# Kernel tuning notes

Hardware: AMD Instinct MI355X
Metric: run time of the kernel (lower is better)

## Reference

```python
import jax, jax.numpy as jnp
import numpy as np

B, N, E, D, H, HW, L = 16, 32, 256, 256, 8, 784, 4
DH = D // H
FF = 4 * D
BN = B * N
BE = B * E
SCALE = 1.0 / np.sqrt(DH)


def _ln(x, g, b):
    m = x.mean(-1, keepdims=True)
    v = ((x - m) ** 2).mean(-1, keepdims=True)
    return (x - m) * jax.lax.rsqrt(v + 1e-5) * g + b


def setup_inputs() -> dict:
    key = jax.random.key(0)
    ks = iter(jax.random.split(key, 64))
    def w(shape, s=0.05):
        return jax.random.normal(next(ks), shape, jnp.float32) * s
    inp = {
        'nodes': w((B, N, D), 1.0),
        'edges': w((B, E, D), 1.0),
        'images': w((B, HW, D), 1.0),
        'mask': jnp.zeros((B * H, N + E, HW), jnp.float32),
        'node_enc': w((BN, D), 1.0),
        'edge_enc': w((BE, D), 1.0),
        'ln1_g': jnp.ones((L, D), jnp.float32), 'ln1_b': jnp.zeros((L, D), jnp.float32),
        'Wqkv': w((L, D, 3 * D)), 'bqkv': jnp.zeros((L, 3 * D), jnp.float32),
        'Wo': w((L, D, D)), 'bo': jnp.zeros((L, D), jnp.float32),
        'ls1': jnp.full((L, D), 0.1, jnp.float32),
        'ln2_g': jnp.ones((L, D), jnp.float32), 'ln2_b': jnp.zeros((L, D), jnp.float32),
        'Wn1': w((L, D, D)), 'bn1': jnp.zeros((L, D), jnp.float32),
        'Wn2': w((L, D, D)), 'bn2': jnp.zeros((L, D), jnp.float32),
        'We': w((L, D, D)), 'be': jnp.zeros((L, D), jnp.float32),
        'attn_p': w((L, H, DH), 1.0),
        'Weo': w((L, D, D)), 'beo': jnp.zeros((L, D), jnp.float32),
        'Wno': w((L, D, D)), 'bno': jnp.zeros((L, D), jnp.float32),
        'ls2': jnp.full((L, D), 0.1, jnp.float32),
        'ln3_g': jnp.ones((L, D), jnp.float32), 'ln3_b': jnp.zeros((L, D), jnp.float32),
        'W1': w((L, D, FF)), 'b1': jnp.zeros((L, FF), jnp.float32),
        'W2': w((L, FF, D)), 'b2': jnp.zeros((L, D), jnp.float32),
        'ls3': jnp.full((L, D), 0.1, jnp.float32),
        'edge_index': jax.random.randint(next(ks), (2, BE), 0, BN, jnp.int32),
    }
    return inp


def reference(nodes, edges, images, mask, node_enc, edge_enc,
              ln1_g, ln1_b, Wqkv, bqkv, Wo, bo, ls1,
              ln2_g, ln2_b, Wn1, bn1, Wn2, bn2, We, be, attn_p, Weo, beo, Wno, bno, ls2,
              ln3_g, ln3_b, W1, b1, W2, b2, ls3, edge_index):
    idx0, idx1 = edge_index[0], edge_index[1]
    ne = jnp.concatenate([nodes, edges], axis=1)  # [B, N+E, D]
    mask4 = mask.reshape(B, H, N + E, HW)
    for l in range(L):
        # cross-attention ne -> images
        ne1n = _ln(ne, ln1_g[l], ln1_b[l])
        q = (ne1n @ Wqkv[l, :, :D] + bqkv[l, :D]).reshape(B, N + E, H, DH)
        k = (images @ Wqkv[l, :, D:2 * D] + bqkv[l, D:2 * D]).reshape(B, HW, H, DH)
        v = (images @ Wqkv[l, :, 2 * D:] + bqkv[l, 2 * D:]).reshape(B, HW, H, DH)
        scores = jnp.einsum('bqhd,bkhd->bhqk', q, k) * SCALE + mask4
        attn = jax.nn.softmax(scores, axis=-1)
        ctx = jnp.einsum('bhqk,bkhd->bqhd', attn, v).reshape(B, N + E, D)
        ne1 = ne + ls1[l] * (ctx @ Wo[l] + bo[l])
        # modified GAT on flattened graph
        ne2n = _ln(ne1, ln2_g[l], ln2_b[l])
        nodes_f = ne2n[:, :N].reshape(BN, D) + node_enc
        edges_f = ne2n[:, N:].reshape(BE, D) + edge_enc
        fn = (nodes_f @ Wn1[l] + bn1[l])[idx0]
        sn = (nodes_f @ Wn2[l] + bn2[l])[idx0]  # NOTE: original code uses edge_index[0] here too
        ep = edges_f @ We[l] + be[l]
        hidden = jax.nn.gelu(fn + sn + ep, approximate=False)  # [BE, D]
        pres = (hidden.reshape(BE, H, DH) * attn_p[l]).sum(-1)  # [BE, H]
        mseg = jax.ops.segment_max(pres, idx0, num_segments=BN)
        expv = jnp.exp(pres - mseg[idx0])
        denom = jax.ops.segment_sum(expv, idx0, num_segments=BN)
        alpha = expv / denom[idx0]  # scatter_softmax over destination nodes
        new_edges = hidden @ Weo[l] + beo[l]
        vals = (nodes_f[idx1] + new_edges) @ Wno[l] + bno[l]
        vals = vals.reshape(BE, H, DH) * alpha[..., None]
        new_nodes = jax.ops.segment_sum(vals.reshape(BE, D), idx0, num_segments=BN)
        gat = jnp.concatenate([new_nodes.reshape(B, N, D), new_edges.reshape(B, E, D)], axis=1)
        ne2 = ne1 + ls2[l] * gat
        # FFN
        ne3n = _ln(ne2, ln3_g[l], ln3_b[l])
        ffn = jax.nn.gelu(ne3n @ W1[l] + b1[l], approximate=False) @ W2[l] + b2[l]
        ne = ne2 + ls3[l] * ffn
    return ne
```

## Files before the change

kernel.cpp:

```cpp
#include <hip/hip_runtime.h>
#include <math.h>

static constexpr int B_  = 16;
static constexpr int N_  = 32;
static constexpr int E_  = 256;
static constexpr int D_  = 256;
static constexpr int H_  = 8;
static constexpr int HW_ = 784;
static constexpr int L_  = 4;
static constexpr int DH_ = 32;
static constexpr int FF_ = 1024;
static constexpr int BN_ = 512;
static constexpr int BE_ = 4096;
static constexpr int NE_ = 288;
#define SCALE_ 0.17677669529663687f

static constexpr size_t LAYER_W = 1114112;
static constexpr size_t OFF_Q   = 0;
static constexpr size_t OFF_K   = 65536;
static constexpr size_t OFF_V   = 131072;
static constexpr size_t OFF_WO  = 196608;
static constexpr size_t OFF_WN1 = 262144;
static constexpr size_t OFF_WN2 = 327680;
static constexpr size_t OFF_WE  = 393216;
static constexpr size_t OFF_WEO = 458752;
static constexpr size_t OFF_WNO = 524288;
static constexpr size_t OFF_W1  = 589824;
static constexpr size_t OFF_W2  = 851968;

typedef __attribute__((ext_vector_type(8))) short bf16x8;
typedef __attribute__((ext_vector_type(4))) float f32x4;

__device__ __forceinline__ float gelu_f(float x) {
    return 0.5f * x * (1.0f + erff(x * 0.7071067811865476f));
}

__device__ __forceinline__ unsigned short f2bf(float x) {
    unsigned u = __float_as_uint(x);
    u += 0x7FFFu + ((u >> 16) & 1u);
    return (unsigned short)(u >> 16);
}
__device__ __forceinline__ unsigned pack2bf(float a, float b) {
    return (unsigned)f2bf(a) | ((unsigned)f2bf(b) << 16);
}
__device__ __forceinline__ float bf2f(unsigned short u) {
    return __uint_as_float(((unsigned)u) << 16);
}


__global__ void concat_kernel(const float* __restrict__ nodes, const float* __restrict__ edges,
                              float* __restrict__ ne) {
    int tid = blockIdx.x * 256 + threadIdx.x;
    int d = tid & 255;
    int row = tid >> 8;
    int b = row / NE_, pos = row % NE_;
    float v = (pos < N_) ? nodes[(size_t)(b * N_ + pos) * D_ + d]
                         : edges[(size_t)(b * E_ + (pos - N_)) * D_ + d];
    ne[tid] = v;
}

__global__ void imgcast_kernel(const float* __restrict__ img, unsigned short* __restrict__ out) {
    int tid = blockIdx.x * 256 + threadIdx.x;
    const float* p = img + (size_t)tid * 8;
    float4 a = *(const float4*)(p);
    float4 b = *(const float4*)(p + 4);
    uint4 o = make_uint4(pack2bf(a.x, a.y), pack2bf(a.z, a.w),
                         pack2bf(b.x, b.y), pack2bf(b.z, b.w));
    *(uint4*)&out[(size_t)tid * 8] = o;
}

__device__ __forceinline__ float ln_row_val(const float* __restrict__ x, int row, int d,
                                            const float* __restrict__ g, const float* __restrict__ bta,
                                            float* sh1, float* sh2) {
    float v = x[(size_t)row * D_ + d];
    float s = v, s2 = v * v;
    #pragma unroll
    for (int o = 32; o >= 1; o >>= 1) { s += __shfl_down(s, o); s2 += __shfl_down(s2, o); }
    int lane = d & 63, w = d >> 6;
    if (lane == 0) { sh1[w] = s; sh2[w] = s2; }
    __syncthreads();
    if (d == 0) {
        float a = sh1[0] + sh1[1] + sh1[2] + sh1[3];
        float c = sh2[0] + sh2[1] + sh2[2] + sh2[3];
        sh1[0] = a; sh2[0] = c;
    }
    __syncthreads();
    float mean = sh1[0] * (1.0f / D_);
    float var  = sh2[0] * (1.0f / D_) - mean * mean;
    float rstd = rsqrtf(var + 1e-5f);
    return (v - mean) * rstd * g[d] + bta[d];
}

__global__ __launch_bounds__(256) void ln_kernel(const float* __restrict__ x,
                                                 unsigned short* __restrict__ y,
                                                 const float* __restrict__ g,
                                                 const float* __restrict__ bta) {
    __shared__ float sh1[4], sh2[4];
    const int row = blockIdx.x, d = threadIdx.x;
    float val = ln_row_val(x, row, d, g, bta, sh1, sh2);
    y[(size_t)row * D_ + d] = f2bf(val);
}

__global__ __launch_bounds__(256) void ln2enc_kernel(const float* __restrict__ x,
                                                     const float* __restrict__ g,
                                                     const float* __restrict__ bta,
                                                     const float* __restrict__ node_enc,
                                                     const float* __restrict__ edge_enc,
                                                     unsigned short* __restrict__ nodes_f,
                                                     unsigned short* __restrict__ edges_f) {
    __shared__ float sh1[4], sh2[4];
    const int row = blockIdx.x, d = threadIdx.x;
    float val = ln_row_val(x, row, d, g, bta, sh1, sh2);
    int b = row / NE_, pos = row % NE_;
    if (pos < N_) {
        int rn = b * N_ + pos;
        nodes_f[(size_t)rn * D_ + d] = f2bf(val + node_enc[(size_t)rn * D_ + d]);
    } else {
        int re = b * E_ + (pos - N_);
        edges_f[(size_t)re * D_ + d] = f2bf(val + edge_enc[(size_t)re * D_ + d]);
    }
}

__global__ __launch_bounds__(256) void wtrans_kernel(
    const float* __restrict__ Wqkv, const float* __restrict__ Wo,
    const float* __restrict__ Wn1,  const float* __restrict__ Wn2,
    const float* __restrict__ We,   const float* __restrict__ Weo,
    const float* __restrict__ Wno,  const float* __restrict__ W1,
    const float* __restrict__ W2,   unsigned short* __restrict__ wT)
{
    const int bid = blockIdx.x;
    const int l = bid / 1088;
    int tl = bid % 1088;
    const float* src; int ld, K, Nn; unsigned short* dst;
    if (tl < 576) {
        int mid = tl >> 6; tl &= 63;
        K = 256; Nn = 256;
        if (mid < 3) {
            src = Wqkv + (size_t)l * 256 * 768 + mid * 256; ld = 768;
            dst = wT + (size_t)l * LAYER_W + (size_t)mid * 65536;
        } else {
            const float* bases[6] = {Wo, Wn1, Wn2, We, Weo, Wno};
            src = bases[mid - 3] + (size_t)l * 65536; ld = 256;
            dst = wT + (size_t)l * LAYER_W + OFF_WO + (size_t)(mid - 3) * 65536;
        }
    } else if (tl < 832) {
        tl -= 576; K = 256; Nn = 1024;
        src = W1 + (size_t)l * 262144; ld = 1024;
        dst = wT + (size_t)l * LAYER_W + OFF_W1;
    } else {
        tl -= 832; K = 1024; Nn = 256;
        src = W2 + (size_t)l * 262144; ld = 256;
        dst = wT + (size_t)l * LAYER_W + OFF_W2;
    }
    const int ntn = Nn >> 5;
    const int k0 = (tl / ntn) << 5, n0 = (tl % ntn) << 5;
    __shared__ float ts[32][33];
    const int t = threadIdx.x;
    const int kl = t >> 5, nl = t & 31;
    #pragma unroll
    for (int rr = 0; rr < 4; ++rr)
        ts[kl + rr * 8][nl] = src[(size_t)(k0 + kl + rr * 8) * ld + n0 + nl];
    __syncthreads();
    const int onl = t >> 3, okl = (t & 7) << 2;
    ushort4 o;
    o.x = f2bf(ts[okl + 0][onl]); o.y = f2bf(ts[okl + 1][onl]);
    o.z = f2bf(ts[okl + 2][onl]); o.w = f2bf(ts[okl + 3][onl]);
    *(ushort4*)&dst[(size_t)(n0 + onl) * K + k0 + okl] = o;
}

template<int MODE, int OUTBF>
__global__ __launch_bounds__(256) void mgemm_kernel(
    const unsigned short* __restrict__ A, int lda,
    const unsigned short* __restrict__ Bt,
    const float* __restrict__ bias,
    const float* __restrict__ res,
    const float* __restrict__ ls,
    void* __restrict__ Cv, int ldc, int K)
{
    __shared__ unsigned short As[64][72];
    __shared__ unsigned short Bs[64][72];
    const int m0 = blockIdx.y * 64, n0 = blockIdx.x * 64;
    const int t = threadIdx.x;
    const int l = t & 63, w = t >> 6;
    const int wr = (w >> 1) * 32, wc = (w & 1) * 32;
    const int srow = t >> 2, skc = (t & 3) * 16;
    const int frow = l & 15, kg = l >> 4;
    f32x4 acc[2][2];
    acc[0][0] = (f32x4){0.f,0.f,0.f,0.f}; acc[0][1] = acc[0][0];
    acc[1][0] = acc[0][0];                acc[1][1] = acc[0][0];
    for (int k0 = 0; k0 < K; k0 += 64) {
        const unsigned short* ap = A + (size_t)(m0 + srow) * lda + k0 + skc;
        uint4 aq0 = *(const uint4*)(ap);
        uint4 aq1 = *(const uint4*)(ap + 8);
        const unsigned short* bp = Bt + (size_t)(n0 + srow) * K + k0 + skc;
        uint4 bq0 = *(const uint4*)(bp);
        uint4 bq1 = *(const uint4*)(bp + 8);
        __syncthreads();
        *(uint4*)&As[srow][skc]     = aq0;
        *(uint4*)&As[srow][skc + 8] = aq1;
        *(uint4*)&Bs[srow][skc]     = bq0;
        *(uint4*)&Bs[srow][skc + 8] = bq1;
        __syncthreads();
        #pragma unroll
        for (int kk = 0; kk < 2; ++kk) {
            bf16x8 af0 = *(const bf16x8*)&As[wr + frow][kk * 32 + kg * 8];
            bf16x8 af1 = *(const bf16x8*)&As[wr + 16 + frow][kk * 32 + kg * 8];
            bf16x8 bf0 = *(const bf16x8*)&Bs[wc + frow][kk * 32 + kg * 8];
            bf16x8 bf1 = *(const bf16x8*)&Bs[wc + 16 + frow][kk * 32 + kg * 8];
            acc[0][0] = __builtin_amdgcn_mfma_f32_16x16x32_bf16(af0, bf0, acc[0][0], 0, 0, 0);
            acc[0][1] = __builtin_amdgcn_mfma_f32_16x16x32_bf16(af0, bf1, acc[0][1], 0, 0, 0);
            acc[1][0] = __builtin_amdgcn_mfma_f32_16x16x32_bf16(af1, bf0, acc[1][0], 0, 0, 0);
            acc[1][1] = __builtin_amdgcn_mfma_f32_16x16x32_bf16(af1, bf1, acc[1][1], 0, 0, 0);
        }
    }
    #pragma unroll
    for (int fr = 0; fr < 2; ++fr) {
        #pragma unroll
        for (int fc = 0; fc < 2; ++fc) {
            int n = n0 + wc + fc * 16 + frow;
            float bv = bias[n];
            float lv = (MODE == 2) ? ls[n] : 0.f;
            #pragma unroll
            for (int rg = 0; rg < 4; ++rg) {
                int m = m0 + wr + fr * 16 + kg * 4 + rg;
                float vv = acc[fr][fc][rg] + bv;
                if (MODE == 1) vv = gelu_f(vv);
                if (MODE == 2) vv = res[(size_t)m * ldc + n] + lv * vv;
                if (OUTBF) ((unsigned short*)Cv)[(size_t)m * ldc + n] = f2bf(vv);
                else       ((float*)Cv)[(size_t)m * ldc + n] = vv;
            }
        }
    }
}

__global__ __launch_bounds__(128) void attn_kernel(
    const unsigned short* __restrict__ q, const unsigned short* __restrict__ kv,
    const float* __restrict__ mask, unsigned short* __restrict__ ctx)
{
    const int bid = blockIdx.x;
    const int h = bid & 7;
    const int qt = (bid >> 3) % 9;
    const int b = (bid >> 3) / 9;
    const int q0 = qt * 32;
    const int t = threadIdx.x;
    const int w = t >> 6, l = t & 63;
    const int lr = l & 15, lg = l >> 4;
    constexpr int NC = (HW_ + 63) / 64;

    __shared__ unsigned short Ks[2][64][40];
    __shared__ unsigned short Vs[2][32][72];
    __shared__ unsigned short Pl[2][16][72];

    bf16x8 qfrag = *(const bf16x8*)(q + ((size_t)(b * NE_ + q0 + w * 16 + lr)) * D_ + h * DH_ + lg * 8);

    const int kkey = t >> 1, kdh = (t & 1) * 16;
    const int vdh = (t & 7) * 4, vk0 = (t >> 3) * 2;
    const unsigned short* kbase = kv + ((size_t)b * HW_) * 512 + h * DH_;
    const unsigned short* vbase = kv + ((size_t)b * HW_) * 512 + 256 + h * DH_;
    const float* mbase = mask + ((size_t)(b * H_ + h) * NE_ + q0 + w * 16 + lg * 4) * (size_t)HW_;

    uint4 kq0, kq1;
    ushort4 va[2], vb4[2];
    float mreg[4][4];

    auto issue_kv = [&](int c0) {
        {
            int key = c0 + kkey;
            bool ok = key < HW_;
            const unsigned short* kp = kbase + (size_t)(ok ? key : 0) * 512 + kdh;
            kq0 = *(const uint4*)(kp);
            kq1 = *(const uint4*)(kp + 8);
            if (!ok) { kq0 = make_uint4(0,0,0,0); kq1 = kq0; }
        }
        #pragma unroll
        for (int r = 0; r < 2; ++r) {
            int key = c0 + vk0 + 32 * r;
            bool ok0 = key < HW_, ok1 = (key + 1) < HW_;
            const unsigned short* vp = vbase + (size_t)(ok0 ? key : 0) * 512 + vdh;
            va[r]  = *(const ushort4*)(vp);
            vb4[r] = *(const ushort4*)(vp + (ok1 ? 512 : 0));
            if (!ok0) va[r]  = make_ushort4(0,0,0,0);
            if (!ok1) vb4[r] = make_ushort4(0,0,0,0);
        }
    };
    auto write_kv = [&](int bufi) {
        *(uint4*)&Ks[bufi][kkey][kdh]     = kq0;
        *(uint4*)&Ks[bufi][kkey][kdh + 8] = kq1;
        #pragma unroll
        for (int r = 0; r < 2; ++r) {
            const unsigned short* a = (const unsigned short*)&va[r];
            const unsigned short* c = (const unsigned short*)&vb4[r];
            #pragma unroll
            for (int i = 0; i < 4; ++i)
                *(unsigned*)&Vs[bufi][vdh + i][vk0 + 32 * r] = (unsigned)a[i] | ((unsigned)c[i] << 16);
        }
    };
    auto issue_mask = [&](int c0) {
        #pragma unroll
        for (int rg = 0; rg < 4; ++rg)
            #pragma unroll
            for (int fc = 0; fc < 4; ++fc) {
                int col = c0 + fc * 16 + lr;
                mreg[rg][fc] = (col < HW_) ? mbase[(size_t)rg * HW_ + col] : -1e30f;
            }
    };

    f32x4 oacc[2];
    oacc[0] = (f32x4){0.f, 0.f, 0.f, 0.f}; oacc[1] = oacc[0];
    float m_i[4] = {-INFINITY, -INFINITY, -INFINITY, -INFINITY};
    float l_i[4] = {0.f, 0.f, 0.f, 0.f};

    issue_kv(0);
    write_kv(0);
    issue_mask(0);
    __syncthreads();

    for (int c = 0; c < NC; ++c) {
        const int c0 = c * 64;
        const int cb = c & 1, nb = cb ^ 1;
        if (c + 1 < NC) issue_kv(c0 + 64);

        f32x4 sacc[4];
        #pragma unroll
        for (int fc = 0; fc < 4; ++fc) {
            sacc[fc] = (f32x4){0.f, 0.f, 0.f, 0.f};
            bf16x8 kf = *(const bf16x8*)&Ks[cb][fc * 16 + lr][lg * 8];
            sacc[fc] = __builtin_amdgcn_mfma_f32_16x16x32_bf16(qfrag, kf, sacc[fc], 0, 0, 0);
        }
        float s[4][4];
        #pragma unroll
        for (int fc = 0; fc < 4; ++fc)
            #pragma unroll
            for (int rg = 0; rg < 4; ++rg)
                s[fc][rg] = sacc[fc][rg] * SCALE_ + mreg[rg][fc];
        if (c + 1 < NC) issue_mask(c0 + 64);

        float mloc[4];
        #pragma unroll
        for (int rg = 0; rg < 4; ++rg)
            mloc[rg] = fmaxf(fmaxf(s[0][rg], s[1][rg]), fmaxf(s[2][rg], s[3][rg]));
        #pragma unroll
        for (int off = 1; off < 16; off <<= 1)
            #pragma unroll
            for (int rg = 0; rg < 4; ++rg)
                mloc[rg] = fmaxf(mloc[rg], __shfl_xor(mloc[rg], off));
        float scl[4], lloc[4];
        #pragma unroll
        for (int rg = 0; rg < 4; ++rg) {
            float mn = fmaxf(m_i[rg], mloc[rg]);
            scl[rg] = __expf(m_i[rg] - mn);
            m_i[rg] = mn;
        }
        #pragma unroll
        for (int rg = 0; rg < 4; ++rg) {
            float acc = 0.f;
            #pragma unroll
            for (int fc = 0; fc < 4; ++fc) {
                float p = __expf(s[fc][rg] - m_i[rg]);
                s[fc][rg] = p;
                acc += p;
            }
            lloc[rg] = acc;
        }
        #pragma unroll
        for (int off = 1; off < 16; off <<= 1)
            #pragma unroll
            for (int rg = 0; rg < 4; ++rg)
                lloc[rg] += __shfl_xor(lloc[rg], off);
        #pragma unroll
        for (int rg = 0; rg < 4; ++rg) {
            l_i[rg] = l_i[rg] * scl[rg] + lloc[rg];
            oacc[0][rg] *= scl[rg];
            oacc[1][rg] *= scl[rg];
        }

        #pragma unroll
        for (int fc = 0; fc < 4; ++fc)
            #pragma unroll
            for (int rg = 0; rg < 4; ++rg)
                Pl[w][lg * 4 + rg][fc * 16 + lr] = f2bf(s[fc][rg]);
        #pragma unroll
        for (int ks2 = 0; ks2 < 2; ++ks2) {
            bf16x8 pf = *(const bf16x8*)&Pl[w][lr][ks2 * 32 + lg * 8];
            #pragma unroll
            for (int d2 = 0; d2 < 2; ++d2) {
                bf16x8 vf = *(const bf16x8*)&Vs[cb][d2 * 16 + lr][ks2 * 32 + lg * 8];
                oacc[d2] = __builtin_amdgcn_mfma_f32_16x16x32_bf16(pf, vf, oacc[d2], 0, 0, 0);
            }
        }

        if (c + 1 < NC) {
            write_kv(nb);
            __syncthreads();
        }
    }

    unsigned short* cbase = ctx + ((size_t)(b * NE_ + q0 + w * 16 + lg * 4)) * D_ + h * DH_;
    #pragma unroll
    for (int rg = 0; rg < 4; ++rg) {
        float inv = 1.0f / l_i[rg];
        #pragma unroll
        for (int d2 = 0; d2 < 2; ++d2)
            cbase[(size_t)rg * D_ + d2 * 16 + lr] = f2bf(oacc[d2][rg] * inv);
    }
}


__global__ __launch_bounds__(256) void hidden_kernel(
    const float* __restrict__ gn1, const float* __restrict__ gn2,
    unsigned short* __restrict__ hid, const int* __restrict__ idx0,
    const float* __restrict__ attn_p_l, float* __restrict__ pres) {
    int e = blockIdx.x;
    int d = threadIdx.x;
    int n = idx0[e];
    float x = bf2f(hid[(size_t)e * D_ + d]) + gn1[(size_t)n * D_ + d] + gn2[(size_t)n * D_ + d];
    float hv = gelu_f(x);
    hid[(size_t)e * D_ + d] = f2bf(hv);
    float pr = hv * attn_p_l[d];
    #pragma unroll
    for (int o = 1; o < 32; o <<= 1) pr += __shfl_xor(pr, o);
    if ((d & 31) == 0) pres[e * H_ + (d >> 5)] = pr;
}

__global__ void segsoft_kernel(const float* __restrict__ pres, const int* __restrict__ csr_off,
                               const int* __restrict__ csr_perm,
                               float* __restrict__ mseg, float* __restrict__ denom) {
    int tid = blockIdx.x * 256 + threadIdx.x;
    int n = tid >> 3, h = tid & 7;
    int s = csr_off[n], e2 = csr_off[n + 1];
    float mx = -INFINITY;
    for (int i = s; i < e2; ++i) mx = fmaxf(mx, pres[csr_perm[i] * H_ + h]);
    float sum = 0.f;
    for (int i = s; i < e2; ++i) sum += expf(pres[csr_perm[i] * H_ + h] - mx);
    mseg[tid] = mx;
    denom[tid] = sum;
}

__global__ void alpha_kernel(const float* __restrict__ pres, const int* __restrict__ idx0,
                             const float* __restrict__ mseg, const float* __restrict__ denom,
                             float* __restrict__ alpha) {
    int tid = blockIdx.x * 256 + threadIdx.x;
    int e = tid >> 3, h = tid & 7;
    int n = idx0[e];
    alpha[tid] = expf(pres[tid] - mseg[n * H_ + h]) / denom[n * H_ + h];
}

__global__ void vin_kernel(const unsigned short* __restrict__ nodes_f,
                           const float* __restrict__ new_edges,
                           const int* __restrict__ idx1, unsigned short* __restrict__ vin) {
    int tid = blockIdx.x * 256 + threadIdx.x;
    int e = tid >> 8, d = tid & 255;
    vin[tid] = f2bf(bf2f(nodes_f[(size_t)idx1[e] * D_ + d]) + new_edges[tid]);
}

__global__ __launch_bounds__(256) void nodeagg_kernel(
    const float* __restrict__ vals, const float* __restrict__ alpha,
    const int* __restrict__ csr_off, const int* __restrict__ csr_perm,
    float* __restrict__ new_nodes) {
    int n = blockIdx.x;
    int d = threadIdx.x;
    int s = csr_off[n], e2 = csr_off[n + 1];
    int h = d >> 5;
    float acc = 0.f;
    for (int i = s; i < e2; ++i) {
        int e = csr_perm[i];
        acc += vals[(size_t)e * D_ + d] * alpha[e * H_ + h];
    }
    new_nodes[(size_t)n * D_ + d] = acc;
}

__global__ void gatres_kernel(float* __restrict__ ne, const float* __restrict__ new_nodes,
                              const float* __restrict__ new_edges, const float* __restrict__ ls2l) {
    int tid = blockIdx.x * 256 + threadIdx.x;
    int d = tid & 255;
    int row = tid >> 8;
    int b = row / NE_, pos = row % NE_;
    float g = (pos < N_) ? new_nodes[(size_t)(b * N_ + pos) * D_ + d]
                         : new_edges[(size_t)(b * E_ + (pos - N_)) * D_ + d];
    ne[tid] += ls2l[d] * g;
}


__global__ void zero_counts(int* counts) {
    int t = blockIdx.x * 256 + threadIdx.x;
    if (t < BN_) counts[t] = 0;
}

__global__ void csr_count(const int* __restrict__ idx0, int* __restrict__ counts) {
    int e = blockIdx.x * 256 + threadIdx.x;
    if (e < BE_) atomicAdd(&counts[idx0[e]], 1);
}

__global__ __launch_bounds__(512) void csr_scan(const int* __restrict__ counts, int* __restrict__ csr_off) {
    __shared__ int buf[BN_];
    int t = threadIdx.x;
    int c = counts[t];
    buf[t] = c;
    __syncthreads();
    for (int o = 1; o < BN_; o <<= 1) {
        int add = (t >= o) ? buf[t - o] : 0;
        __syncthreads();
        buf[t] += add;
        __syncthreads();
    }
    csr_off[t] = buf[t] - c;
    if (t == BN_ - 1) csr_off[BN_] = buf[t];
}

__global__ __launch_bounds__(64) void csr_fill(const int* __restrict__ idx0,
                                               const int* __restrict__ csr_off,
                                               int* __restrict__ csr_perm) {
    int n = blockIdx.x;
    int lane = threadIdx.x;
    int w = csr_off[n];
    for (int c0 = 0; c0 < BE_; c0 += 64) {
        int e = c0 + lane;
        bool m = (idx0[e] == n);
        unsigned long long bal = __ballot(m);
        if (m) {
            int pre = __popcll(bal & ((1ull << lane) - 1ull));
            csr_perm[w + pre] = e;
        }
        w += __popcll(bal);
    }
}


static void launch_mgemm(hipStream_t s, int mode, int outbf,
                         const unsigned short* A, int lda, const unsigned short* Bt,
                         const float* bias, const float* res, const float* ls,
                         void* C, int ldc, int M, int N, int K) {
    dim3 g(N / 64, M / 64);
    if (mode == 0) {
        if (outbf) mgemm_kernel<0,1><<<g, 256, 0, s>>>(A, lda, Bt, bias, res, ls, C, ldc, K);
        else       mgemm_kernel<0,0><<<g, 256, 0, s>>>(A, lda, Bt, bias, res, ls, C, ldc, K);
    } else if (mode == 1) {
        mgemm_kernel<1,1><<<g, 256, 0, s>>>(A, lda, Bt, bias, res, ls, C, ldc, K);
    } else {
        mgemm_kernel<2,0><<<g, 256, 0, s>>>(A, lda, Bt, bias, res, ls, C, ldc, K);
    }
}

extern "C" void kernel_launch(void* const* d_in, const int* in_sizes, int n_in,
                              void* d_out, int out_size, void* d_ws, size_t ws_size,
                              hipStream_t stream) {
    const float* nodes    = (const float*)d_in[0];
    const float* edges    = (const float*)d_in[1];
    const float* images   = (const float*)d_in[2];
    const float* mask     = (const float*)d_in[3];
    const float* node_enc = (const float*)d_in[4];
    const float* edge_enc = (const float*)d_in[5];
    const float* ln1_g = (const float*)d_in[6];
    const float* ln1_b = (const float*)d_in[7];
    const float* Wqkv  = (const float*)d_in[8];
    const float* bqkv  = (const float*)d_in[9];
    const float* Wo    = (const float*)d_in[10];
    const float* bo    = (const float*)d_in[11];
    const float* ls1   = (const float*)d_in[12];
    const float* ln2_g = (const float*)d_in[13];
    const float* ln2_b = (const float*)d_in[14];
    const float* Wn1   = (const float*)d_in[15];
    const float* bn1   = (const float*)d_in[16];
    const float* Wn2   = (const float*)d_in[17];
    const float* bn2   = (const float*)d_in[18];
    const float* We    = (const float*)d_in[19];
    const float* be    = (const float*)d_in[20];
    const float* attn_p= (const float*)d_in[21];
    const float* Weo   = (const float*)d_in[22];
    const float* beo   = (const float*)d_in[23];
    const float* Wno   = (const float*)d_in[24];
    const float* bno   = (const float*)d_in[25];
    const float* ls2   = (const float*)d_in[26];
    const float* ln3_g = (const float*)d_in[27];
    const float* ln3_b = (const float*)d_in[28];
    const float* W1    = (const float*)d_in[29];
    const float* b1    = (const float*)d_in[30];
    const float* W2    = (const float*)d_in[31];
    const float* b2    = (const float*)d_in[32];
    const float* ls3   = (const float*)d_in[33];
    const int*   edge_index = (const int*)d_in[34];
    const int* idx0 = edge_index;
    const int* idx1 = edge_index + BE_;

    float* ne = (float*)d_out;

    float* cur = (float*)d_ws;
    auto alloc = [&](size_t nfl) { float* p = cur; cur += nfl; return p; };
    auto allocbf = [&](size_t nbf) { float* p = cur; cur += (nbf + 1) / 2; return (unsigned short*)p; };

    unsigned short* lnbuf   = allocbf((size_t)B_ * NE_ * D_);
    unsigned short* qb      = allocbf((size_t)B_ * NE_ * D_);
    unsigned short* kvb     = allocbf((size_t)B_ * HW_ * 512);
    unsigned short* imgbf   = allocbf((size_t)B_ * HW_ * D_);
    unsigned short* ctxb    = allocbf((size_t)B_ * NE_ * D_);
    unsigned short* ffnh    = allocbf((size_t)B_ * NE_ * FF_);
    unsigned short* nodes_f = allocbf((size_t)BN_ * D_);
    unsigned short* edges_f = allocbf((size_t)BE_ * D_);
    unsigned short* hid     = allocbf((size_t)BE_ * D_);
    unsigned short* vin     = allocbf((size_t)BE_ * D_);
    float* gn1      = alloc((size_t)BN_ * D_);
    float* gn2      = alloc((size_t)BN_ * D_);
    float* pres     = alloc((size_t)BE_ * H_);
    float* mseg     = alloc((size_t)BN_ * H_);
    float* denom    = alloc((size_t)BN_ * H_);
    float* alphab   = alloc((size_t)BE_ * H_);
    float* new_edges= alloc((size_t)BE_ * D_);
    float* valsb    = alloc((size_t)BE_ * D_);
    float* new_nodes= alloc((size_t)BN_ * D_);
    int* counts   = (int*)cur; cur += BN_;
    int* csr_off  = (int*)cur; cur += BN_ + 4;
    int* csr_perm = (int*)cur; cur += BE_;
    cur = (float*)(((uintptr_t)cur + 255) & ~(uintptr_t)255);
    unsigned short* wT = (unsigned short*)cur;

    wtrans_kernel<<<4 * 1088, 256, 0, stream>>>(Wqkv, Wo, Wn1, Wn2, We, Weo, Wno, W1, W2, wT);
    imgcast_kernel<<<(B_ * HW_ * D_) / (256 * 8), 256, 0, stream>>>(images, imgbf);
    zero_counts<<<2, 256, 0, stream>>>(counts);
    csr_count<<<BE_ / 256, 256, 0, stream>>>(idx0, counts);
    csr_scan<<<1, 512, 0, stream>>>(counts, csr_off);
    csr_fill<<<BN_, 64, 0, stream>>>(idx0, csr_off, csr_perm);
    concat_kernel<<<(B_ * NE_ * D_) / 256, 256, 0, stream>>>(nodes, edges, ne);

    for (int l = 0; l < L_; ++l) {
        const unsigned short* wTl = wT + (size_t)l * LAYER_W;
        const float* bqkv_l = bqkv + (size_t)l * 3 * D_;

        ln_kernel<<<B_ * NE_, 256, 0, stream>>>(ne, lnbuf, ln1_g + l * D_, ln1_b + l * D_);
        launch_mgemm(stream, 0, 1, lnbuf, D_, wTl + OFF_Q, bqkv_l, nullptr, nullptr,
                     qb, D_, B_ * NE_, D_, D_);
        launch_mgemm(stream, 0, 1, imgbf, D_, wTl + OFF_K, bqkv_l + D_, nullptr, nullptr,
                     kvb, 512, B_ * HW_, 512, D_);
        attn_kernel<<<1152, 128, 0, stream>>>(qb, kvb, mask, ctxb);
        launch_mgemm(stream, 2, 0, ctxb, D_, wTl + OFF_WO, bo + l * D_, ne, ls1 + l * D_,
                     ne, D_, B_ * NE_, D_, D_);

        ln2enc_kernel<<<B_ * NE_, 256, 0, stream>>>(ne, ln2_g + l * D_, ln2_b + l * D_,
                                                    node_enc, edge_enc, nodes_f, edges_f);
        launch_mgemm(stream, 0, 0, nodes_f, D_, wTl + OFF_WN1, bn1 + l * D_, nullptr, nullptr,
                     gn1, D_, BN_, D_, D_);
        launch_mgemm(stream, 0, 0, nodes_f, D_, wTl + OFF_WN2, bn2 + l * D_, nullptr, nullptr,
                     gn2, D_, BN_, D_, D_);
        launch_mgemm(stream, 0, 1, edges_f, D_, wTl + OFF_WE, be + l * D_, nullptr, nullptr,
                     hid, D_, BE_, D_, D_);
        hidden_kernel<<<BE_, 256, 0, stream>>>(gn1, gn2, hid, idx0, attn_p + (size_t)l * H_ * DH_, pres);
        segsoft_kernel<<<(BN_ * H_) / 256, 256, 0, stream>>>(pres, csr_off, csr_perm, mseg, denom);
        alpha_kernel<<<(BE_ * H_) / 256, 256, 0, stream>>>(pres, idx0, mseg, denom, alphab);
        launch_mgemm(stream, 0, 0, hid, D_, wTl + OFF_WEO, beo + l * D_, nullptr, nullptr,
                     new_edges, D_, BE_, D_, D_);
        vin_kernel<<<(BE_ * D_) / 256, 256, 0, stream>>>(nodes_f, new_edges, idx1, vin);
        launch_mgemm(stream, 0, 0, vin, D_, wTl + OFF_WNO, bno + l * D_, nullptr, nullptr,
                     valsb, D_, BE_, D_, D_);
        nodeagg_kernel<<<BN_, 256, 0, stream>>>(valsb, alphab, csr_off, csr_perm, new_nodes);
        gatres_kernel<<<(B_ * NE_ * D_) / 256, 256, 0, stream>>>(ne, new_nodes, new_edges, ls2 + l * D_);

        ln_kernel<<<B_ * NE_, 256, 0, stream>>>(ne, lnbuf, ln3_g + l * D_, ln3_b + l * D_);
        launch_mgemm(stream, 1, 1, lnbuf, D_, wTl + OFF_W1, b1 + l * FF_, nullptr, nullptr,
                     ffnh, FF_, B_ * NE_, FF_, D_);
        launch_mgemm(stream, 2, 0, ffnh, FF_, wTl + OFF_W2, b2 + l * D_, ne, ls3 + l * D_,
                     ne, D_, B_ * NE_, D_, FF_);
    }
}
```

Before: 688.2 us.

## Coalesce mask loads via LDS, merge node GEMMs, fuse alpha and gatres+LN

The attention mask is now loaded with coalesced float4 reads, converted to bf16 into a double-buffered LDS tile, and prefetched with K/V. The two node projections run as one wider GEMM with a second bias. The alpha computation moves into node aggregation, the GAT residual is fused with LN3, and the FFN hidden buffer reuses the KV buffer. Together these cut global memory traffic and kernel launches, at the cost of bf16 rounding of mask values and extra LDS use in attention.

```diff
diff --git a/kernel.cpp b/kernel.cpp
--- a/kernel.cpp
+++ b/kernel.cpp
@@ -18,10 +18,8 @@
 static constexpr size_t LAYER_W = 1114112;
 static constexpr size_t OFF_Q   = 0;
 static constexpr size_t OFF_K   = 65536;
-static constexpr size_t OFF_V   = 131072;
 static constexpr size_t OFF_WO  = 196608;
 static constexpr size_t OFF_WN1 = 262144;
-static constexpr size_t OFF_WN2 = 327680;
 static constexpr size_t OFF_WE  = 393216;
 static constexpr size_t OFF_WEO = 458752;
 static constexpr size_t OFF_WNO = 524288;
@@ -69,10 +67,9 @@
     *(uint4*)&out[(size_t)tid * 8] = o;
 }
 
-__device__ __forceinline__ float ln_row_val(const float* __restrict__ x, int row, int d,
-                                            const float* __restrict__ g, const float* __restrict__ bta,
-                                            float* sh1, float* sh2) {
-    float v = x[(size_t)row * D_ + d];
+__device__ __forceinline__ float ln_from_val(float v, int d,
+                                             const float* __restrict__ g, const float* __restrict__ bta,
+                                             float* sh1, float* sh2) {
     float s = v, s2 = v * v;
     #pragma unroll
     for (int o = 32; o >= 1; o >>= 1) { s += __shfl_down(s, o); s2 += __shfl_down(s2, o); }
@@ -97,8 +94,8 @@
                                                  const float* __restrict__ bta) {
     __shared__ float sh1[4], sh2[4];
     const int row = blockIdx.x, d = threadIdx.x;
-    float val = ln_row_val(x, row, d, g, bta, sh1, sh2);
-    y[(size_t)row * D_ + d] = f2bf(val);
+    float v = x[(size_t)row * D_ + d];
+    y[(size_t)row * D_ + d] = f2bf(ln_from_val(v, d, g, bta, sh1, sh2));
 }
 
 __global__ __launch_bounds__(256) void ln2enc_kernel(const float* __restrict__ x,
@@ -110,7 +107,8 @@
                                                      unsigned short* __restrict__ edges_f) {
     __shared__ float sh1[4], sh2[4];
     const int row = blockIdx.x, d = threadIdx.x;
-    float val = ln_row_val(x, row, d, g, bta, sh1, sh2);
+    float v = x[(size_t)row * D_ + d];
+    float val = ln_from_val(v, d, g, bta, sh1, sh2);
     int b = row / NE_, pos = row % NE_;
     if (pos < N_) {
         int rn = b * N_ + pos;
@@ -119,6 +117,21 @@
         int re = b * E_ + (pos - N_);
         edges_f[(size_t)re * D_ + d] = f2bf(val + edge_enc[(size_t)re * D_ + d]);
     }
+}
+
+__global__ __launch_bounds__(256) void gatres_ln_kernel(
+    float* __restrict__ ne, const float* __restrict__ new_nodes,
+    const float* __restrict__ new_edges, const float* __restrict__ ls2l,
+    const float* __restrict__ g, const float* __restrict__ bta,
+    unsigned short* __restrict__ lnb) {
+    __shared__ float sh1[4], sh2[4];
+    const int row = blockIdx.x, d = threadIdx.x;
+    int b = row / NE_, pos = row % NE_;
+    float gv = (pos < N_) ? new_nodes[(size_t)(b * N_ + pos) * D_ + d]
+                          : new_edges[(size_t)(b * E_ + (pos - N_)) * D_ + d];
+    float v = ne[(size_t)row * D_ + d] + ls2l[d] * gv;
+    ne[(size_t)row * D_ + d] = v;
+    lnb[(size_t)row * D_ + d] = f2bf(ln_from_val(v, d, g, bta, sh1, sh2));
 }
 
 __global__ __launch_bounds__(256) void wtrans_kernel(
@@ -173,6 +186,7 @@
     const unsigned short* __restrict__ A, int lda,
     const unsigned short* __restrict__ Bt,
     const float* __restrict__ bias,
+    const float* __restrict__ bias2,
     const float* __restrict__ res,
     const float* __restrict__ ls,
     void* __restrict__ Cv, int ldc, int K)
@@ -218,7 +232,7 @@
         #pragma unroll
         for (int fc = 0; fc < 2; ++fc) {
             int n = n0 + wc + fc * 16 + frow;
-            float bv = bias[n];
+            float bv = (bias2 != nullptr && n >= 256) ? bias2[n - 256] : bias[n];
             float lv = (MODE == 2) ? ls[n] : 0.f;
             #pragma unroll
             for (int rg = 0; rg < 4; ++rg) {
@@ -250,18 +264,20 @@
     __shared__ unsigned short Ks[2][64][40];
     __shared__ unsigned short Vs[2][32][72];
     __shared__ unsigned short Pl[2][16][72];
+    __shared__ unsigned short Msk[2][32][68];
 
     bf16x8 qfrag = *(const bf16x8*)(q + ((size_t)(b * NE_ + q0 + w * 16 + lr)) * D_ + h * DH_ + lg * 8);
 
     const int kkey = t >> 1, kdh = (t & 1) * 16;
     const int vdh = (t & 7) * 4, vk0 = (t >> 3) * 2;
+    const int mrow = t >> 2, mcg = (t & 3) * 16;
     const unsigned short* kbase = kv + ((size_t)b * HW_) * 512 + h * DH_;
     const unsigned short* vbase = kv + ((size_t)b * HW_) * 512 + 256 + h * DH_;
-    const float* mbase = mask + ((size_t)(b * H_ + h) * NE_ + q0 + w * 16 + lg * 4) * (size_t)HW_;
+    const float* mbase = mask + ((size_t)(b * H_ + h) * NE_ + q0 + mrow) * (size_t)HW_;
 
     uint4 kq0, kq1;
     ushort4 va[2], vb4[2];
-    float mreg[4][4];
+    float mf[16];
 
     auto issue_kv = [&](int c0) {
         {
@@ -283,6 +299,22 @@
             if (!ok1) vb4[r] = make_ushort4(0,0,0,0);
         }
     };
+    auto issue_mask = [&](int c0) {
+        if (c0 + 64 <= HW_) {
+            #pragma unroll
+            for (int i = 0; i < 4; ++i) {
+                float4 m4 = *(const float4*)(mbase + c0 + mcg + i * 4);
+                mf[i * 4 + 0] = m4.x; mf[i * 4 + 1] = m4.y;
+                mf[i * 4 + 2] = m4.z; mf[i * 4 + 3] = m4.w;
+            }
+        } else {
+            #pragma unroll
+            for (int i = 0; i < 16; ++i) {
+                int col = c0 + mcg + i;
+                mf[i] = (col < HW_) ? mbase[col] : -1e30f;
+            }
+        }
+    };
     auto write_kv = [&](int bufi) {
         *(uint4*)&Ks[bufi][kkey][kdh]     = kq0;
         *(uint4*)&Ks[bufi][kkey][kdh + 8] = kq1;
@@ -295,14 +327,13 @@
                 *(unsigned*)&Vs[bufi][vdh + i][vk0 + 32 * r] = (unsigned)a[i] | ((unsigned)c[i] << 16);
         }
     };
-    auto issue_mask = [&](int c0) {
-        #pragma unroll
-        for (int rg = 0; rg < 4; ++rg)
-            #pragma unroll
-            for (int fc = 0; fc < 4; ++fc) {
-                int col = c0 + fc * 16 + lr;
-                mreg[rg][fc] = (col < HW_) ? mbase[(size_t)rg * HW_ + col] : -1e30f;
-            }
+    auto write_mask = [&](int bufi) {
+        uint4 p0 = make_uint4(pack2bf(mf[0], mf[1]),  pack2bf(mf[2], mf[3]),
+                              pack2bf(mf[4], mf[5]),  pack2bf(mf[6], mf[7]));
+        uint4 p1 = make_uint4(pack2bf(mf[8], mf[9]),  pack2bf(mf[10], mf[11]),
+                              pack2bf(mf[12], mf[13]), pack2bf(mf[14], mf[15]));
+        *(uint4*)&Msk[bufi][mrow][mcg]     = p0;
+        *(uint4*)&Msk[bufi][mrow][mcg + 8] = p1;
     };
 
     f32x4 oacc[2];
@@ -311,14 +342,15 @@
     float l_i[4] = {0.f, 0.f, 0.f, 0.f};
 
     issue_kv(0);
+    issue_mask(0);
     write_kv(0);
-    issue_mask(0);
+    write_mask(0);
     __syncthreads();
 
     for (int c = 0; c < NC; ++c) {
         const int c0 = c * 64;
         const int cb = c & 1, nb = cb ^ 1;
-        if (c + 1 < NC) issue_kv(c0 + 64);
+        if (c + 1 < NC) { issue_kv(c0 + 64); issue_mask(c0 + 64); }
 
         f32x4 sacc[4];
         #pragma unroll
@@ -332,8 +364,7 @@
         for (int fc = 0; fc < 4; ++fc)
             #pragma unroll
             for (int rg = 0; rg < 4; ++rg)
-                s[fc][rg] = sacc[fc][rg] * SCALE_ + mreg[rg][fc];
-        if (c + 1 < NC) issue_mask(c0 + 64);
+                s[fc][rg] = sacc[fc][rg] * SCALE_ + bf2f(Msk[cb][w * 16 + lg * 4 + rg][fc * 16 + lr]);
 
         float mloc[4];
         #pragma unroll
@@ -391,6 +422,7 @@
 
         if (c + 1 < NC) {
             write_kv(nb);
+            write_mask(nb);
             __syncthreads();
         }
     }
@@ -407,13 +439,13 @@
 
 
 __global__ __launch_bounds__(256) void hidden_kernel(
-    const float* __restrict__ gn1, const float* __restrict__ gn2,
+    const float* __restrict__ gn12,
     unsigned short* __restrict__ hid, const int* __restrict__ idx0,
     const float* __restrict__ attn_p_l, float* __restrict__ pres) {
     int e = blockIdx.x;
     int d = threadIdx.x;
     int n = idx0[e];
-    float x = bf2f(hid[(size_t)e * D_ + d]) + gn1[(size_t)n * D_ + d] + gn2[(size_t)n * D_ + d];
+    float x = bf2f(hid[(size_t)e * D_ + d]) + gn12[(size_t)n * 512 + d] + gn12[(size_t)n * 512 + 256 + d];
     float hv = gelu_f(x);
     hid[(size_t)e * D_ + d] = f2bf(hv);
     float pr = hv * attn_p_l[d];
@@ -436,15 +468,6 @@
     denom[tid] = sum;
 }
 
-__global__ void alpha_kernel(const float* __restrict__ pres, const int* __restrict__ idx0,
-                             const float* __restrict__ mseg, const float* __restrict__ denom,
-                             float* __restrict__ alpha) {
-    int tid = blockIdx.x * 256 + threadIdx.x;
-    int e = tid >> 3, h = tid & 7;
-    int n = idx0[e];
-    alpha[tid] = expf(pres[tid] - mseg[n * H_ + h]) / denom[n * H_ + h];
-}
-
 __global__ void vin_kernel(const unsigned short* __restrict__ nodes_f,
                            const float* __restrict__ new_edges,
                            const int* __restrict__ idx1, unsigned short* __restrict__ vin) {
@@ -454,30 +477,23 @@
 }
 
 __global__ __launch_bounds__(256) void nodeagg_kernel(
-    const float* __restrict__ vals, const float* __restrict__ alpha,
+    const float* __restrict__ vals, const float* __restrict__ pres,
+    const float* __restrict__ mseg, const float* __restrict__ denom,
     const int* __restrict__ csr_off, const int* __restrict__ csr_perm,
     float* __restrict__ new_nodes) {
     int n = blockIdx.x;
     int d = threadIdx.x;
     int s = csr_off[n], e2 = csr_off[n + 1];
     int h = d >> 5;
+    float ms = mseg[n * H_ + h];
+    float rd = 1.0f / denom[n * H_ + h];
     float acc = 0.f;
     for (int i = s; i < e2; ++i) {
         int e = csr_perm[i];
-        acc += vals[(size_t)e * D_ + d] * alpha[e * H_ + h];
+        float a = expf(pres[e * H_ + h] - ms) * rd;
+        acc += vals[(size_t)e * D_ + d] * a;
     }
     new_nodes[(size_t)n * D_ + d] = acc;
-}
-
-__global__ void gatres_kernel(float* __restrict__ ne, const float* __restrict__ new_nodes,
-                              const float* __restrict__ new_edges, const float* __restrict__ ls2l) {
-    int tid = blockIdx.x * 256 + threadIdx.x;
-    int d = tid & 255;
-    int row = tid >> 8;
-    int b = row / NE_, pos = row % NE_;
-    float g = (pos < N_) ? new_nodes[(size_t)(b * N_ + pos) * D_ + d]
-                         : new_edges[(size_t)(b * E_ + (pos - N_)) * D_ + d];
-    ne[tid] += ls2l[d] * g;
 }
 
 
@@ -528,16 +544,16 @@
 
 static void launch_mgemm(hipStream_t s, int mode, int outbf,
                          const unsigned short* A, int lda, const unsigned short* Bt,
-                         const float* bias, const float* res, const float* ls,
+                         const float* bias, const float* bias2, const float* res, const float* ls,
                          void* C, int ldc, int M, int N, int K) {
     dim3 g(N / 64, M / 64);
     if (mode == 0) {
-        if (outbf) mgemm_kernel<0,1><<<g, 256, 0, s>>>(A, lda, Bt, bias, res, ls, C, ldc, K);
-        else       mgemm_kernel<0,0><<<g, 256, 0, s>>>(A, lda, Bt, bias, res, ls, C, ldc, K);
+        if (outbf) mgemm_kernel<0,1><<<g, 256, 0, s>>>(A, lda, Bt, bias, bias2, res, ls, C, ldc, K);
+        else       mgemm_kernel<0,0><<<g, 256, 0, s>>>(A, lda, Bt, bias, bias2, res, ls, C, ldc, K);
     } else if (mode == 1) {
-        mgemm_kernel<1,1><<<g, 256, 0, s>>>(A, lda, Bt, bias, res, ls, C, ldc, K);
+        mgemm_kernel<1,1><<<g, 256, 0, s>>>(A, lda, Bt, bias, bias2, res, ls, C, ldc, K);
     } else {
-        mgemm_kernel<2,0><<<g, 256, 0, s>>>(A, lda, Bt, bias, res, ls, C, ldc, K);
+        mgemm_kernel<2,0><<<g, 256, 0, s>>>(A, lda, Bt, bias, bias2, res, ls, C, ldc, K);
     }
 }
 
@@ -591,19 +607,17 @@
     unsigned short* lnbuf   = allocbf((size_t)B_ * NE_ * D_);
     unsigned short* qb      = allocbf((size_t)B_ * NE_ * D_);
     unsigned short* kvb     = allocbf((size_t)B_ * HW_ * 512);
+    unsigned short* ffnh    = kvb;
     unsigned short* imgbf   = allocbf((size_t)B_ * HW_ * D_);
     unsigned short* ctxb    = allocbf((size_t)B_ * NE_ * D_);
-    unsigned short* ffnh    = allocbf((size_t)B_ * NE_ * FF_);
     unsigned short* nodes_f = allocbf((size_t)BN_ * D_);
     unsigned short* edges_f = allocbf((size_t)BE_ * D_);
     unsigned short* hid     = allocbf((size_t)BE_ * D_);
     unsigned short* vin     = allocbf((size_t)BE_ * D_);
-    float* gn1      = alloc((size_t)BN_ * D_);
-    float* gn2      = alloc((size_t)BN_ * D_);
+    float* gn12     = alloc((size_t)BN_ * 512);
     float* pres     = alloc((size_t)BE_ * H_);
     float* mseg     = alloc((size_t)BN_ * H_);
     float* denom    = alloc((size_t)BN_ * H_);
-    float* alphab   = alloc((size_t)BE_ * H_);
     float* new_edges= alloc((size_t)BE_ * D_);
     float* valsb    = alloc((size_t)BE_ * D_);
     float* new_nodes= alloc((size_t)BN_ * D_);
@@ -626,37 +640,34 @@
         const float* bqkv_l = bqkv + (size_t)l * 3 * D_;
 
         ln_kernel<<<B_ * NE_, 256, 0, stream>>>(ne, lnbuf, ln1_g + l * D_, ln1_b + l * D_);
-        launch_mgemm(stream, 0, 1, lnbuf, D_, wTl + OFF_Q, bqkv_l, nullptr, nullptr,
+        launch_mgemm(stream, 0, 1, lnbuf, D_, wTl + OFF_Q, bqkv_l, nullptr, nullptr, nullptr,
                      qb, D_, B_ * NE_, D_, D_);
-        launch_mgemm(stream, 0, 1, imgbf, D_, wTl + OFF_K, bqkv_l + D_, nullptr, nullptr,
+        launch_mgemm(stream, 0, 1, imgbf, D_, wTl + OFF_K, bqkv_l + D_, nullptr, nullptr, nullptr,
                      kvb, 512, B_ * HW_, 512, D_);
         attn_kernel<<<1152, 128, 0, stream>>>(qb, kvb, mask, ctxb);
-        launch_mgemm(stream, 2, 0, ctxb, D_, wTl + OFF_WO, bo + l * D_, ne, ls1 + l * D_,
+        launch_mgemm(stream, 2, 0, ctxb, D_, wTl + OFF_WO, bo + l * D_, nullptr, ne, ls1 + l * D_,
                      ne, D_, B_ * NE_, D_, D_);
 
         ln2enc_kernel<<<B_ * NE_, 256, 0, stream>>>(ne, ln2_g + l * D_, ln2_b + l * D_,
                                                     node_enc, edge_enc, nodes_f, edges_f);
-        launch_mgemm(stream, 0, 0, nodes_f, D_, wTl + OFF_WN1, bn1 + l * D_, nullptr, nullptr,
-                     gn1, D_, BN_, D_, D_);
-        launch_mgemm(stream, 0, 0, nodes_f, D_, wTl + OFF_WN2, bn2 + l * D_, nullptr, nullptr,
-                     gn2, D_, BN_, D_, D_);
-        launch_mgemm(stream, 0, 1, edges_f, D_, wTl + OFF_WE, be + l * D_, nullptr, nullptr,
+        launch_mgemm(stream, 0, 0, nodes_f, D_, wTl + OFF_WN1, bn1 + l * D_, bn2 + l * D_,
+                     nullptr, nullptr, gn12, 512, BN_, 512, D_);
+        launch_mgemm(stream, 0, 1, edges_f, D_, wTl + OFF_WE, be + l * D_, nullptr, nullptr, nullptr,
                      hid, D_, BE_, D_, D_);
-        hidden_kernel<<<BE_, 256, 0, stream>>>(gn1, gn2, hid, idx0, attn_p + (size_t)l * H_ * DH_, pres);
+        hidden_kernel<<<BE_, 256, 0, stream>>>(gn12, hid, idx0, attn_p + (size_t)l * H_ * DH_, pres);
         segsoft_kernel<<<(BN_ * H_) / 256, 256, 0, stream>>>(pres, csr_off, csr_perm, mseg, denom);
-        alpha_kernel<<<(BE_ * H_) / 256, 256, 0, stream>>>(pres, idx0, mseg, denom, alphab);
-        launch_mgemm(stream, 0, 0, hid, D_, wTl + OFF_WEO, beo + l * D_, nullptr, nullptr,
+        launch_mgemm(stream, 0, 0, hid, D_, wTl + OFF_WEO, beo + l * D_, nullptr, nullptr, nullptr,
                      new_edges, D_, BE_, D_, D_);
         vin_kernel<<<(BE_ * D_) / 256, 256, 0, stream>>>(nodes_f, new_edges, idx1, vin);
-        launch_mgemm(stream, 0, 0, vin, D_, wTl + OFF_WNO, bno + l * D_, nullptr, nullptr,
+        launch_mgemm(stream, 0, 0, vin, D_, wTl + OFF_WNO, bno + l * D_, nullptr, nullptr, nullptr,
                      valsb, D_, BE_, D_, D_);
-        nodeagg_kernel<<<BN_, 256, 0, stream>>>(valsb, alphab, csr_off, csr_perm, new_nodes);
-        gatres_kernel<<<(B_ * NE_ * D_) / 256, 256, 0, stream>>>(ne, new_nodes, new_edges, ls2 + l * D_);
-
-        ln_kernel<<<B_ * NE_, 256, 0, stream>>>(ne, lnbuf, ln3_g + l * D_, ln3_b + l * D_);
-        launch_mgemm(stream, 1, 1, lnbuf, D_, wTl + OFF_W1, b1 + l * FF_, nullptr, nullptr,
+        nodeagg_kernel<<<BN_, 256, 0, stream>>>(valsb, pres, mseg, denom, csr_off, csr_perm, new_nodes);
+        gatres_ln_kernel<<<B_ * NE_, 256, 0, stream>>>(ne, new_nodes, new_edges, ls2 + l * D_,
+                                                       ln3_g + l * D_, ln3_b + l * D_, lnbuf);
+
+        launch_mgemm(stream, 1, 1, lnbuf, D_, wTl + OFF_W1, b1 + l * FF_, nullptr, nullptr, nullptr,
                      ffnh, FF_, B_ * NE_, FF_, D_);
-        launch_mgemm(stream, 2, 0, ffnh, FF_, wTl + OFF_W2, b2 + l * D_, ne, ls3 + l * D_,
+        launch_mgemm(stream, 2, 0, ffnh, FF_, wTl + OFF_W2, b2 + l * D_, nullptr, ne, ls3 + l * D_,
                      ne, D_, B_ * NE_, D_, FF_);
     }
 }
```

Result: no change. 675.8 us (-1.8%).
